# Performance work log

Hardware: AMD Instinct MI355X
Metric: run time of the kernel (lower is better)

## Reference

```python
import jax, jax.numpy as jnp
import numpy as np

N = 100_000   # nodes
E = 1_600_000 # edges
F_IN = 256    # num_features
HID = 128     # hidden_channels * heads
G = 128       # graphs in batch
C = 2         # num_classes
BN_EPS = 1e-5


def setup_inputs() -> dict:
    key = jax.random.key(0)
    ks = jax.random.split(key, 12)
    x = jax.random.normal(ks[0], (N, F_IN), dtype=jnp.float32)
    edge_index = jax.random.randint(ks[1], (2, E), 0, N, dtype=jnp.int64)
    batch = jnp.sort(jax.random.randint(ks[2], (N,), 0, G, dtype=jnp.int64))
    s1 = 1.0 / np.sqrt(F_IN)
    s2 = 1.0 / np.sqrt(HID)
    W1 = jax.random.uniform(ks[3], (F_IN, HID), jnp.float32, -s1, s1)
    b1 = jnp.zeros((HID,), jnp.float32)
    W2 = jax.random.uniform(ks[4], (HID, HID), jnp.float32, -s2, s2)
    b2 = jnp.zeros((HID,), jnp.float32)
    W3 = jax.random.uniform(ks[5], (HID, HID), jnp.float32, -s2, s2)
    b3 = jnp.zeros((HID,), jnp.float32)
    bn_gamma = jnp.ones((HID,), jnp.float32)
    bn_beta = jnp.zeros((HID,), jnp.float32)
    bn_mean = jnp.zeros((HID,), jnp.float32)
    bn_var = jnp.ones((HID,), jnp.float32)
    lin_w = jax.random.uniform(ks[6], (HID, C), jnp.float32, -s2, s2)
    lin_b = jax.random.uniform(ks[7], (C,), jnp.float32, -s2, s2)
    return {
        "x": x, "edge_index": edge_index, "_": 0, "batch": batch,
        "W1": W1, "b1": b1, "W2": W2, "b2": b2, "W3": W3, "b3": b3,
        "bn_gamma": bn_gamma, "bn_beta": bn_beta,
        "bn_mean": bn_mean, "bn_var": bn_var,
        "lin_w": lin_w, "lin_b": lin_b,
    }


def reference(x, edge_index, _, batch, W1, b1, W2, b2, W3, b3,
              bn_gamma, bn_beta, bn_mean, bn_var, lin_w, lin_b):
    src, dst = edge_index[0], edge_index[1]
    # GCN symmetric normalization with self-loops (gcn_norm):
    # deg[i] = 1 + in_degree(i); norm_e = deg[src]^-1/2 * deg[dst]^-1/2
    deg = 1.0 + jax.ops.segment_sum(jnp.ones((E,), x.dtype), dst, num_segments=N)
    dis = jax.lax.rsqrt(deg)
    norm_e = (dis[src] * dis[dst])[:, None]        # [E,1]
    self_norm = (1.0 / deg)[:, None]               # [N,1] self-loop weight

    def gcn_conv(h, W, b):
        hw = h @ W                                  # transform first (PyG order)
        agg = jax.ops.segment_sum(hw[src] * norm_e, dst, num_segments=N)
        return agg + hw * self_norm + b

    h = jax.nn.relu(gcn_conv(x, W1, b1))
    h = jax.nn.relu(gcn_conv(h, W2, b2))
    h = jax.nn.relu(gcn_conv(h, W3, b3))

    # global_mean_pool over graph ids
    counts = jax.ops.segment_sum(jnp.ones((N,), h.dtype), batch, num_segments=G)
    pooled = jax.ops.segment_sum(h, batch, num_segments=G) / jnp.maximum(counts, 1.0)[:, None]

    # dropout p=0.5 is identity in eval mode; BatchNorm1d with running stats
    xb = (pooled - bn_mean) * jax.lax.rsqrt(bn_var + BN_EPS) * bn_gamma + bn_beta
    out = jax.nn.relu(xb @ lin_w + lin_b)
    return (xb, out)
```

## Files before the change

### kernel.cpp

```cpp
#include <hip/hip_runtime.h>

#define NNODES 100000
#define NEDGES 1600000
#define FIN 256
#define HID 128
#define NG 128
#define NB 391
#define NW 256
#define EPW 6250
#define GEMM_BLKS 1563

static constexpr float BN_EPS_C = 1e-5f;

typedef __attribute__((ext_vector_type(8))) short bf16x8;
typedef __attribute__((ext_vector_type(4))) float f32x4;
typedef __attribute__((ext_vector_type(2))) float f32x2;

#if defined(__has_builtin)
#if __has_builtin(__builtin_amdgcn_cvt_pk_f32_fp8)
#define HAS_HWFP8 1
#endif
#endif

__device__ __forceinline__ float b2f(unsigned short u) {
    union { unsigned int i; float f; } c; c.i = ((unsigned int)u) << 16; return c.f;
}
__device__ __forceinline__ unsigned short f2b(float f) {
    union { float f; unsigned int i; } c; c.f = f;
    unsigned int u = c.i;
    u += 0x7fffu + ((u >> 16) & 1u);
    return (unsigned short)(u >> 16);
}

__device__ __forceinline__ unsigned char f2e8(float f) {
    union { float f; unsigned int u; } c; c.f = f;
    unsigned int s = (c.u >> 24) & 0x80u;
    c.u &= 0x7fffffffu;
    c.f = fminf(fmaxf(c.f, 0.015625f), 448.f);
    unsigned int u = c.u + 0x7ffffu + ((c.u >> 20) & 1u);
    int e = (int)(u >> 23) - 127;
    unsigned int m = (u >> 20) & 7u;
    return (unsigned char)(s | ((unsigned int)(e + 7) << 3) | m);
}

__device__ __forceinline__ float e8byte(unsigned int b) {
    union { unsigned int u; float f; } c;
    c.u = ((b & 0x80u) << 24) | (0x3C000000u + ((b & 0x7fu) << 20));
    return c.f;
}
__device__ __forceinline__ f32x2 e8plo(unsigned int w) {
#ifdef HAS_HWFP8
    return __builtin_amdgcn_cvt_pk_f32_fp8(w, false);
#else
    f32x2 r; r[0] = e8byte(w & 0xffu); r[1] = e8byte((w >> 8) & 0xffu); return r;
#endif
}
__device__ __forceinline__ f32x2 e8phi(unsigned int w) {
#ifdef HAS_HWFP8
    return __builtin_amdgcn_cvt_pk_f32_fp8(w, true);
#else
    f32x2 r; r[0] = e8byte((w >> 16) & 0xffu); r[1] = e8byte(w >> 24); return r;
#endif
}
__device__ __forceinline__ f32x2 bdec(unsigned int u) {
    union { unsigned int i[2]; f32x2 f; } c;
    c.i[0] = u << 16;
    c.i[1] = u & 0xffff0000u;
    return c.f;
}

__device__ __forceinline__ int aswz(int g) { return g ^ ((g >> 4) & 3); }

template<int K, int MODE, int OUT8>
__device__ __forceinline__ void gemm_body(int blk,
                                          const void* __restrict__ Araw,
                                          const unsigned short* __restrict__ whl,
                                          void* __restrict__ hwbv) {
    __shared__ __align__(16) unsigned short Ah0[2048];
    __shared__ __align__(16) unsigned short Ah1[2048];
    __shared__ __align__(16) unsigned short Bs[8192];

    const int tid = threadIdx.x;
    const int w = tid >> 6;
    const int lane = tid & 63;
    const int m0 = blk * 64;
    const int ar = tid >> 2;
    const int ak = (tid & 3) * 8;
    const int adst = aswz(((ar >> 4) * 64) + (ar & 15) + 16 * (ak >> 3)) * 8;
    const int ards = aswz(w * 64 + lane) * 8;

    f32x4 acc[8] = {};

    for (int kt = 0; kt < K; kt += 32) {
        if (MODE == 0) {
            const float* A = (const float*)Araw;
            float4 v0 = {0.f,0.f,0.f,0.f}, v1 = {0.f,0.f,0.f,0.f};
            int grow = m0 + ar;
            if (grow < NNODES) {
                const float* s = A + (size_t)grow * K + kt + ak;
                v0 = *(const float4*)(s);
                v1 = *(const float4*)(s + 4);
            }
            float av[8];
            *(float4*)(av) = v0; *(float4*)(av + 4) = v1;
            bf16x8 hv, lv;
            #pragma unroll
            for (int j = 0; j < 8; ++j) {
                unsigned short h = f2b(av[j]);
                hv[j] = (short)h;
                lv[j] = (short)f2b(av[j] - b2f(h));
            }
            *(bf16x8*)&Ah0[adst] = hv;
            *(bf16x8*)&Ah1[adst] = lv;
        } else {
            const unsigned short* A = (const unsigned short*)Araw;
            bf16x8 hv = {};
            int grow = m0 + ar;
            if (grow < NNODES)
                hv = *(const bf16x8*)(A + (size_t)grow * K + kt + ak);
            *(bf16x8*)&Ah0[adst] = hv;
        }
        {
            const float4* bsrc = (const float4*)(whl + (size_t)(kt >> 5) * 8192);
            float4* bdst = (float4*)Bs;
            #pragma unroll
            for (int i = 0; i < 4; ++i) bdst[tid * 4 + i] = bsrc[tid * 4 + i];
        }
        __syncthreads();
        bf16x8 a0 = *(const bf16x8*)&Ah0[ards];
        bf16x8 a1;
        if (MODE == 0) a1 = *(const bf16x8*)&Ah1[ards];
        #pragma unroll
        for (int t = 0; t < 8; ++t) {
            bf16x8 b0 = *(const bf16x8*)&Bs[(t * 64 + lane) * 8];
            bf16x8 b1 = *(const bf16x8*)&Bs[4096 + (t * 64 + lane) * 8];
            acc[t] = __builtin_amdgcn_mfma_f32_16x16x32_bf16(a0, b0, acc[t], 0, 0, 0);
            acc[t] = __builtin_amdgcn_mfma_f32_16x16x32_bf16(a0, b1, acc[t], 0, 0, 0);
            if (MODE == 0)
                acc[t] = __builtin_amdgcn_mfma_f32_16x16x32_bf16(a1, b0, acc[t], 0, 0, 0);
        }
        __syncthreads();
    }

    const int colLo = lane & 15;
    const int gq = lane >> 4;
    #pragma unroll
    for (int i = 0; i < 4; ++i) {
        int row = m0 + w * 16 + gq * 4 + i;
        if (row < NNODES) {
            #pragma unroll
            for (int t = 0; t < 8; ++t) {
                int col = t * 16 + colLo;
                float v = acc[t][i];
                if (OUT8) {
                    ((unsigned char*)hwbv)[(size_t)row * HID + col] = f2e8(v * 64.f);
                } else {
                    ((unsigned short*)hwbv)[(size_t)row * HID + col] = f2b(v);
                }
            }
        }
    }
}

__global__ __launch_bounds__(256) void k_prep(const float* __restrict__ W1,
                                              const float* __restrict__ W2,
                                              const float* __restrict__ W3,
                                              unsigned short* __restrict__ whl1,
                                              unsigned short* __restrict__ whl2,
                                              unsigned short* __restrict__ whl3,
                                              const int* __restrict__ dst,
                                              int* __restrict__ hist) {
    if (blockIdx.x < 256) {
        int idx = blockIdx.x * 256 + threadIdx.x;
        const float* W; unsigned short* whl;
        if (idx < FIN * 128) { W = W1; whl = whl1; }
        else if (idx < (FIN + HID) * 128) { W = W2; whl = whl2; idx -= FIN * 128; }
        else { W = W3; whl = whl3; idx -= (FIN + HID) * 128; }
        int k = idx >> 7, c = idx & 127;
        float v = W[k * 128 + c];
        unsigned short hi = f2b(v);
        unsigned short lo = f2b(v - b2f(hi));
        int kstep = k >> 5, kk = k & 31, g = kk >> 3, j = kk & 7;
        int tile = c >> 4, lane = (c & 15) + 16 * g;
        size_t b0 = ((((size_t)kstep * 2 + 0) * 8 + tile) * 64 + lane) * 8 + j;
        size_t b1 = ((((size_t)kstep * 2 + 1) * 8 + tile) * 64 + lane) * 8 + j;
        whl[b0] = hi;
        whl[b1] = lo;
    } else {
        __shared__ int h[NB];
        int w = blockIdx.x - 256, t = threadIdx.x;
        for (int i = t; i < NB; i += 256) h[i] = 0;
        __syncthreads();
        int base = w * EPW;
        for (int i = t; i < EPW; i += 256) atomicAdd(&h[dst[base + i] >> 8], 1);
        __syncthreads();
        for (int i = t; i < NB; i += 256) hist[i * NW + w] = h[i];
    }
}

__global__ __launch_bounds__(256) void kbB2(const int* __restrict__ hist,
                                            int* __restrict__ off,
                                            int* __restrict__ btot) {
    __shared__ int s[NW];
    int b = blockIdx.x, t = threadIdx.x;
    int v = hist[b * NW + t];
    s[t] = v;
    __syncthreads();
    for (int o = 1; o < NW; o <<= 1) {
        int a = (t >= o) ? s[t - o] : 0;
        __syncthreads();
        s[t] += a;
        __syncthreads();
    }
    off[b * NW + t] = s[t] - v;
    if (t == NW - 1) btot[b] = s[t];
}

__global__ __launch_bounds__(512) void kbT(const int* __restrict__ btot,
                                           int* __restrict__ bbase,
                                           int* __restrict__ rowptr) {
    __shared__ int s[512];
    int t = threadIdx.x;
    int v = (t < NB) ? btot[t] : 0;
    s[t] = v;
    __syncthreads();
    for (int o = 1; o < 512; o <<= 1) {
        int a = (t >= o) ? s[t - o] : 0;
        __syncthreads();
        s[t] += a;
        __syncthreads();
    }
    if (t < NB) bbase[t] = s[t] - v;
    if (t == NB - 1) { bbase[NB] = s[t]; rowptr[NNODES] = NEDGES; }
}

__global__ __launch_bounds__(256) void k_c2g1(const int* __restrict__ src,
                                              const int* __restrict__ dst,
                                              const int* __restrict__ off,
                                              const int* __restrict__ bbase,
                                              int* __restrict__ pairs,
                                              const float* __restrict__ x,
                                              const unsigned short* __restrict__ whl1,
                                              void* __restrict__ hwbv) {
    if (blockIdx.x < 256) {
        __shared__ int cur[NB];
        int w = blockIdx.x, t = threadIdx.x;
        for (int i = t; i < NB; i += 256) cur[i] = off[i * NW + w] + bbase[i];
        __syncthreads();
        int base = w * EPW;
        for (int i = t; i < EPW; i += 256) {
            int d = dst[base + i];
            int pos = atomicAdd(&cur[d >> 8], 1);
            pairs[pos] = (src[base + i] << 8) | (d & 255);
        }
    } else {
        gemm_body<FIN, 0, 1>(blockIdx.x - 256, x, whl1, hwbv);
    }
}

__global__ __launch_bounds__(256) void kb2y(const int* __restrict__ bbase,
                                            const int* __restrict__ pairs,
                                            int* __restrict__ rowptr,
                                            float* __restrict__ dis,
                                            float* __restrict__ selfn) {
    int b = blockIdx.x;
    int nbase = b * 256;
    int nmax = NNODES - nbase; if (nmax > 256) nmax = 256;
    __shared__ int cnt[256];
    __shared__ int cur[256];
    int t = threadIdx.x;
    cnt[t] = 0;
    __syncthreads();
    int beg = bbase[b], end = bbase[b + 1];
    for (int i = beg + t; i < end; i += 256) atomicAdd(&cnt[pairs[i] & 255], 1);
    __syncthreads();
    int v = cnt[t];
    cur[t] = v;
    __syncthreads();
    for (int o = 1; o < 256; o <<= 1) {
        int a = (t >= o) ? cur[t - o] : 0;
        __syncthreads();
        cur[t] += a;
        __syncthreads();
    }
    if (t < nmax) {
        rowptr[nbase + t] = cur[t] - v + beg;
        float d = 1.0f + (float)v;
        dis[nbase + t] = rsqrtf(d);
        selfn[nbase + t] = 1.0f / d;
    }
}

__global__ __launch_bounds__(256) void kb2z(const int* __restrict__ bbase,
                                            const int* __restrict__ pairs,
                                            const int* __restrict__ rowptr,
                                            const float* __restrict__ dis,
                                            unsigned int* __restrict__ edgp) {
    int b = blockIdx.x;
    int nbase = b * 256;
    int nmax = NNODES - nbase; if (nmax > 256) nmax = 256;
    __shared__ int cur[256];
    __shared__ float disl[256];
    int t = threadIdx.x;
    if (t < nmax) {
        cur[t] = rowptr[nbase + t];
        disl[t] = dis[nbase + t];
    }
    __syncthreads();
    int beg = bbase[b], end = bbase[b + 1];
    for (int i = beg + t; i < end; i += 256) {
        int p = pairs[i];
        int s = p >> 8;
        float w = dis[s] * disl[p & 255];
        unsigned int u = (unsigned int)(w * 32767.f + 0.5f);
        int pos = atomicAdd(&cur[p & 255], 1);
        edgp[pos] = ((unsigned int)s << 15) | u;
    }
}

template<int K, int MODE, int OUT8>
__global__ __launch_bounds__(256) void k_gemm_mfma(const void* __restrict__ Araw,
                                                   const unsigned short* __restrict__ whl,
                                                   void* __restrict__ hwbv) {
    gemm_body<K, MODE, OUT8>(blockIdx.x, Araw, whl, hwbv);
}

template<int IN8>
__global__ __launch_bounds__(256) void k_gather(const int* __restrict__ rowptr,
                                                const unsigned int* __restrict__ edgp,
                                                const void* __restrict__ hwbv,
                                                const float* __restrict__ selfn,
                                                const float* __restrict__ bias,
                                                unsigned short* __restrict__ agb) {
    const int lane = threadIdx.x & 63;
    const int sub = lane >> 4;
    const int l4 = lane & 15;
    const int node = blockIdx.x * 16 + ((threadIdx.x >> 6) << 2) + sub;
    int beg = rowptr[node], end = rowptr[node + 1];
    const float q = IN8 ? (1.0f / (32767.0f * 64.0f)) : (1.0f / 32767.0f);
    const unsigned char* hb = (const unsigned char*)hwbv;
    f32x2 a0 = {0.f,0.f}, a1 = {0.f,0.f}, a2 = {0.f,0.f}, a3 = {0.f,0.f};
    int e = beg;
    if (IN8) {
        for (; e + 7 < end; e += 8) {
            unsigned int p0 = edgp[e], p1 = edgp[e + 1];
            unsigned int p2 = edgp[e + 2], p3 = edgp[e + 3];
            unsigned int p4 = edgp[e + 4], p5 = edgp[e + 5];
            unsigned int p6 = edgp[e + 6], p7 = edgp[e + 7];
            uint2 v0 = *(const uint2*)(hb + (size_t)(p0 >> 15) * HID + l4 * 8);
            uint2 v1 = *(const uint2*)(hb + (size_t)(p1 >> 15) * HID + l4 * 8);
            uint2 v2 = *(const uint2*)(hb + (size_t)(p2 >> 15) * HID + l4 * 8);
            uint2 v3 = *(const uint2*)(hb + (size_t)(p3 >> 15) * HID + l4 * 8);
            uint2 v4 = *(const uint2*)(hb + (size_t)(p4 >> 15) * HID + l4 * 8);
            uint2 v5 = *(const uint2*)(hb + (size_t)(p5 >> 15) * HID + l4 * 8);
            uint2 v6 = *(const uint2*)(hb + (size_t)(p6 >> 15) * HID + l4 * 8);
            uint2 v7 = *(const uint2*)(hb + (size_t)(p7 >> 15) * HID + l4 * 8);
            float w0 = (float)(p0 & 0x7fffu) * q, w1 = (float)(p1 & 0x7fffu) * q;
            float w2 = (float)(p2 & 0x7fffu) * q, w3 = (float)(p3 & 0x7fffu) * q;
            float w4 = (float)(p4 & 0x7fffu) * q, w5 = (float)(p5 & 0x7fffu) * q;
            float w6 = (float)(p6 & 0x7fffu) * q, w7 = (float)(p7 & 0x7fffu) * q;
            f32x2 wa = {w0, w0}, wb = {w1, w1}, wc = {w2, w2}, wd = {w3, w3};
            f32x2 we = {w4, w4}, wf = {w5, w5}, wg = {w6, w6}, wh = {w7, w7};
            a0 += e8plo(v0.x) * wa; a1 += e8phi(v0.x) * wa;
            a2 += e8plo(v0.y) * wa; a3 += e8phi(v0.y) * wa;
            a0 += e8plo(v1.x) * wb; a1 += e8phi(v1.x) * wb;
            a2 += e8plo(v1.y) * wb; a3 += e8phi(v1.y) * wb;
            a0 += e8plo(v2.x) * wc; a1 += e8phi(v2.x) * wc;
            a2 += e8plo(v2.y) * wc; a3 += e8phi(v2.y) * wc;
            a0 += e8plo(v3.x) * wd; a1 += e8phi(v3.x) * wd;
            a2 += e8plo(v3.y) * wd; a3 += e8phi(v3.y) * wd;
            a0 += e8plo(v4.x) * we; a1 += e8phi(v4.x) * we;
            a2 += e8plo(v4.y) * we; a3 += e8phi(v4.y) * we;
            a0 += e8plo(v5.x) * wf; a1 += e8phi(v5.x) * wf;
            a2 += e8plo(v5.y) * wf; a3 += e8phi(v5.y) * wf;
            a0 += e8plo(v6.x) * wg; a1 += e8phi(v6.x) * wg;
            a2 += e8plo(v6.y) * wg; a3 += e8phi(v6.y) * wg;
            a0 += e8plo(v7.x) * wh; a1 += e8phi(v7.x) * wh;
            a2 += e8plo(v7.y) * wh; a3 += e8phi(v7.y) * wh;
        }
    } else {
        for (; e + 3 < end; e += 4) {
            unsigned int p0 = edgp[e], p1 = edgp[e + 1];
            unsigned int p2 = edgp[e + 2], p3 = edgp[e + 3];
            float w0 = (float)(p0 & 0x7fffu) * q;
            float w1 = (float)(p1 & 0x7fffu) * q;
            float w2 = (float)(p2 & 0x7fffu) * q;
            float w3 = (float)(p3 & 0x7fffu) * q;
            f32x2 wa = {w0, w0}, wb = {w1, w1}, wc = {w2, w2}, wd = {w3, w3};
            size_t r0 = (size_t)(p0 >> 15), r1 = (size_t)(p1 >> 15);
            size_t r2 = (size_t)(p2 >> 15), r3 = (size_t)(p3 >> 15);
            uint4 v0 = *(const uint4*)(hb + r0 * (HID * 2) + l4 * 16);
            uint4 v1 = *(const uint4*)(hb + r1 * (HID * 2) + l4 * 16);
            uint4 v2 = *(const uint4*)(hb + r2 * (HID * 2) + l4 * 16);
            uint4 v3 = *(const uint4*)(hb + r3 * (HID * 2) + l4 * 16);
            a0 += bdec(v0.x) * wa; a1 += bdec(v0.y) * wa;
            a2 += bdec(v0.z) * wa; a3 += bdec(v0.w) * wa;
            a0 += bdec(v1.x) * wb; a1 += bdec(v1.y) * wb;
            a2 += bdec(v1.z) * wb; a3 += bdec(v1.w) * wb;
            a0 += bdec(v2.x) * wc; a1 += bdec(v2.y) * wc;
            a2 += bdec(v2.z) * wc; a3 += bdec(v2.w) * wc;
            a0 += bdec(v3.x) * wd; a1 += bdec(v3.y) * wd;
            a2 += bdec(v3.z) * wd; a3 += bdec(v3.w) * wd;
        }
    }
    for (; e < end; ++e) {
        unsigned int p = edgp[e];
        float w = (float)(p & 0x7fffu) * q;
        f32x2 wa = {w, w};
        size_t r = (size_t)(p >> 15);
        if (IN8) {
            uint2 v = *(const uint2*)(hb + r * HID + l4 * 8);
            a0 += e8plo(v.x) * wa; a1 += e8phi(v.x) * wa;
            a2 += e8plo(v.y) * wa; a3 += e8phi(v.y) * wa;
        } else {
            uint4 v = *(const uint4*)(hb + r * (HID * 2) + l4 * 16);
            a0 += bdec(v.x) * wa; a1 += bdec(v.y) * wa;
            a2 += bdec(v.z) * wa; a3 += bdec(v.w) * wa;
        }
    }
    float sn = selfn[node] * (IN8 ? (1.0f / 64.0f) : 1.0f);
    f32x2 sn2 = {sn, sn};
    f32x2 h0, h1, h2, h3;
    if (IN8) {
        uint2 v = *(const uint2*)(hb + (size_t)node * HID + l4 * 8);
        h0 = e8plo(v.x); h1 = e8phi(v.x); h2 = e8plo(v.y); h3 = e8phi(v.y);
    } else {
        uint4 v = *(const uint4*)(hb + (size_t)node * (HID * 2) + l4 * 16);
        h0 = bdec(v.x); h1 = bdec(v.y); h2 = bdec(v.z); h3 = bdec(v.w);
    }
    float4 bA = *(const float4*)&bias[l4 * 8];
    float4 bB = *(const float4*)&bias[l4 * 8 + 4];
    a0 += h0 * sn2; a1 += h1 * sn2; a2 += h2 * sn2; a3 += h3 * sn2;
    float r0 = fmaxf(a0[0] + bA.x, 0.f), r1 = fmaxf(a0[1] + bA.y, 0.f);
    float r2 = fmaxf(a1[0] + bA.z, 0.f), r3 = fmaxf(a1[1] + bA.w, 0.f);
    float r4 = fmaxf(a2[0] + bB.x, 0.f), r5 = fmaxf(a2[1] + bB.y, 0.f);
    float r6 = fmaxf(a3[0] + bB.z, 0.f), r7 = fmaxf(a3[1] + bB.w, 0.f);
    uint4 o;
    o.x = (unsigned int)f2b(r0) | ((unsigned int)f2b(r1) << 16);
    o.y = (unsigned int)f2b(r2) | ((unsigned int)f2b(r3) << 16);
    o.z = (unsigned int)f2b(r4) | ((unsigned int)f2b(r5) << 16);
    o.w = (unsigned int)f2b(r6) | ((unsigned int)f2b(r7) << 16);
    *(uint4*)(agb + (size_t)node * HID + l4 * 8) = o;
}

__global__ __launch_bounds__(1024) void k_pool_bn_head(const unsigned short* __restrict__ h,
                                                       const int* __restrict__ batch,
                                                       const float* __restrict__ gamma,
                                                       const float* __restrict__ beta,
                                                       const float* __restrict__ mean,
                                                       const float* __restrict__ var,
                                                       const float* __restrict__ lw,
                                                       const float* __restrict__ lb,
                                                       float* __restrict__ xb,
                                                       float* __restrict__ out2) {
    int g = blockIdx.x;
    int tid = threadIdx.x;
    int fg = tid & 15;
    int r = tid >> 4;
    __shared__ int bounds[2];
    if (tid < 2) {
        int target = g + tid;
        int a = 0, b = NNODES;
        while (a < b) { int m = (a + b) >> 1; if (batch[m] < target) a = m + 1; else b = m; }
        bounds[tid] = a;
    }
    __syncthreads();
    int s1 = bounds[0], e1 = bounds[1];
    f32x2 acc[4] = {};
    for (int i = s1 + r; i < e1; i += 64) {
        uint4 v = *(const uint4*)(h + (size_t)i * HID + fg * 8);
        acc[0] += bdec(v.x); acc[1] += bdec(v.y); acc[2] += bdec(v.z); acc[3] += bdec(v.w);
    }
    __shared__ f32x2 red[64][16][4];
    #pragma unroll
    for (int j = 0; j < 4; ++j) red[r][fg][j] = acc[j];
    __syncthreads();
    for (int off = 32; off >= 1; off >>= 1) {
        if (r < off) {
            #pragma unroll
            for (int j = 0; j < 4; ++j) red[r][fg][j] += red[r + off][fg][j];
        }
        __syncthreads();
    }
    __shared__ float xbl[128];
    if (r == 0) {
        float cnt = (float)((e1 - s1) > 0 ? (e1 - s1) : 1);
        float inv = 1.0f / cnt;
        #pragma unroll
        for (int j = 0; j < 4; ++j) {
            #pragma unroll
            for (int k2 = 0; k2 < 2; ++k2) {
                int f = fg * 8 + j * 2 + k2;
                float pooled = red[0][fg][j][k2] * inv;
                float xbv = (pooled - mean[f]) * rsqrtf(var[f] + BN_EPS_C) * gamma[f] + beta[f];
                xb[g * HID + f] = xbv;
                xbl[f] = xbv;
            }
        }
    }
    __syncthreads();
    if (tid < 64) {
        float x0 = xbl[tid], x1 = xbl[tid + 64];
        float s0 = x0 * lw[tid * 2 + 0] + x1 * lw[(tid + 64) * 2 + 0];
        float s1h = x0 * lw[tid * 2 + 1] + x1 * lw[(tid + 64) * 2 + 1];
        #pragma unroll
        for (int o = 1; o < 64; o <<= 1) {
            s0 += __shfl_xor(s0, o);
            s1h += __shfl_xor(s1h, o);
        }
        if (tid == 0) {
            out2[g * 2 + 0] = fmaxf(s0 + lb[0], 0.f);
            out2[g * 2 + 1] = fmaxf(s1h + lb[1], 0.f);
        }
    }
}

extern "C" void kernel_launch(void* const* d_in, const int* in_sizes, int n_in,
                              void* d_out, int out_size, void* d_ws, size_t ws_size,
                              hipStream_t stream) {
    const float* x     = (const float*)d_in[0];
    const int*   ei    = (const int*)d_in[1];
    const int*   batch = (const int*)d_in[3];
    const float* W1 = (const float*)d_in[4];
    const float* b1 = (const float*)d_in[5];
    const float* W2 = (const float*)d_in[6];
    const float* b2 = (const float*)d_in[7];
    const float* W3 = (const float*)d_in[8];
    const float* b3 = (const float*)d_in[9];
    const float* gamma = (const float*)d_in[10];
    const float* beta  = (const float*)d_in[11];
    const float* mean  = (const float*)d_in[12];
    const float* var   = (const float*)d_in[13];
    const float* lw = (const float*)d_in[14];
    const float* lb = (const float*)d_in[15];
    float* out = (float*)d_out;

    char* p = (char*)d_ws;
    unsigned short* HWB = (unsigned short*)p;          p += (size_t)NNODES * HID * 2;
    unsigned short* AGB = (unsigned short*)p;          p += (size_t)NNODES * HID * 2;
    float* DIS    = (float*)p;                         p += (size_t)NNODES * 4;
    float* SELFN  = (float*)p;                         p += (size_t)NNODES * 4;
    int*   ROWPTR = (int*)p;                           p += (size_t)(NNODES + 64) * 4;
    unsigned int* EDGP = (unsigned int*)p;             p += (size_t)NEDGES * 4;
    int*   PAIRS  = (int*)p;                           p += (size_t)NEDGES * 4;
    int*   BTOT   = (int*)p;                           p += 512 * 4;
    int*   BBASE  = (int*)p;                           p += 512 * 4;
    unsigned short* WHL1 = (unsigned short*)p;         p += (size_t)FIN * 128 * 2 * 2;
    unsigned short* WHL2 = (unsigned short*)p;         p += (size_t)HID * 128 * 2 * 2;
    unsigned short* WHL3 = (unsigned short*)p;
    int*   HIST   = (int*)AGB;
    int*   OFF    = HIST + NB * NW;

    const int* srcv = ei;
    const int* dstv = ei + NEDGES;

    k_prep<<<512, 256, 0, stream>>>(W1, W2, W3, WHL1, WHL2, WHL3, dstv, HIST);
    kbB2<<<NB, 256, 0, stream>>>(HIST, OFF, BTOT);
    kbT<<<1, 512, 0, stream>>>(BTOT, BBASE, ROWPTR);
    k_c2g1<<<256 + GEMM_BLKS, 256, 0, stream>>>(srcv, dstv, OFF, BBASE, PAIRS, x, WHL1, HWB);
    kb2y<<<NB, 256, 0, stream>>>(BBASE, PAIRS, ROWPTR, DIS, SELFN);
    kb2z<<<NB, 256, 0, stream>>>(BBASE, PAIRS, ROWPTR, DIS, EDGP);

    const int ggat = NNODES / 16;
    dim3 gg(GEMM_BLKS);

    k_gather<1><<<ggat, 256, 0, stream>>>(ROWPTR, EDGP, HWB, SELFN, b1, AGB);
    k_gemm_mfma<HID, 1, 1><<<gg, 256, 0, stream>>>(AGB, WHL2, HWB);
    k_gather<1><<<ggat, 256, 0, stream>>>(ROWPTR, EDGP, HWB, SELFN, b2, AGB);
    k_gemm_mfma<HID, 1, 0><<<gg, 256, 0, stream>>>(AGB, WHL3, HWB);
    k_gather<0><<<ggat, 256, 0, stream>>>(ROWPTR, EDGP, HWB, SELFN, b3, AGB);

    k_pool_bn_head<<<NG, 1024, 0, stream>>>(AGB, batch, gamma, beta, mean, var,
                                            lw, lb, out, out + (size_t)NG * HID);
}
```

Baseline: 260.4 us.

## Use single-pass bf16 GEMM for layer 1 and interleave scatter blocks with GEMM blocks

Adds a MODE 2 GEMM path for the first layer that converts x to bf16 once and issues one MFMA per tile. It drops the hi/lo split of A and the second weight half, cutting MFMA count and LDS traffic by about two thirds. It also spreads the 256 edge-scatter blocks evenly among the GEMM blocks (every 7th block) rather than placing them first, so the two workloads share the CUs more evenly. Dropping the compensation terms lowers layer-1 precision, which risks accuracy against the fp32 reference.

```diff
diff --git a/kernel.cpp b/kernel.cpp
--- a/kernel.cpp
+++ b/kernel.cpp
@@ -77,8 +77,8 @@
                                           const unsigned short* __restrict__ whl,
                                           void* __restrict__ hwbv) {
     __shared__ __align__(16) unsigned short Ah0[2048];
-    __shared__ __align__(16) unsigned short Ah1[2048];
-    __shared__ __align__(16) unsigned short Bs[8192];
+    __shared__ __align__(16) unsigned short Ah1[(MODE == 0) ? 2048 : 16];
+    __shared__ __align__(16) unsigned short Bs[(MODE == 2) ? 4096 : 8192];
 
     const int tid = threadIdx.x;
     const int w = tid >> 6;
@@ -92,7 +92,7 @@
     f32x4 acc[8] = {};
 
     for (int kt = 0; kt < K; kt += 32) {
-        if (MODE == 0) {
+        if (MODE == 0 || MODE == 2) {
             const float* A = (const float*)Araw;
             float4 v0 = {0.f,0.f,0.f,0.f}, v1 = {0.f,0.f,0.f,0.f};
             int grow = m0 + ar;
@@ -103,15 +103,17 @@
             }
             float av[8];
             *(float4*)(av) = v0; *(float4*)(av + 4) = v1;
-            bf16x8 hv, lv;
+            bf16x8 hv;
             #pragma unroll
-            for (int j = 0; j < 8; ++j) {
-                unsigned short h = f2b(av[j]);
-                hv[j] = (short)h;
-                lv[j] = (short)f2b(av[j] - b2f(h));
+            for (int j = 0; j < 8; ++j) hv[j] = (short)f2b(av[j]);
+            *(bf16x8*)&Ah0[adst] = hv;
+            if (MODE == 0) {
+                bf16x8 lv;
+                #pragma unroll
+                for (int j = 0; j < 8; ++j)
+                    lv[j] = (short)f2b(av[j] - b2f((unsigned short)hv[j]));
+                *(bf16x8*)&Ah1[adst] = lv;
             }
-            *(bf16x8*)&Ah0[adst] = hv;
-            *(bf16x8*)&Ah1[adst] = lv;
         } else {
             const unsigned short* A = (const unsigned short*)Araw;
             bf16x8 hv = {};
@@ -123,8 +125,13 @@
         {
             const float4* bsrc = (const float4*)(whl + (size_t)(kt >> 5) * 8192);
             float4* bdst = (float4*)Bs;
-            #pragma unroll
-            for (int i = 0; i < 4; ++i) bdst[tid * 4 + i] = bsrc[tid * 4 + i];
+            if (MODE == 2) {
+                #pragma unroll
+                for (int i = 0; i < 2; ++i) bdst[tid * 2 + i] = bsrc[tid * 2 + i];
+            } else {
+                #pragma unroll
+                for (int i = 0; i < 4; ++i) bdst[tid * 4 + i] = bsrc[tid * 4 + i];
+            }
         }
         __syncthreads();
         bf16x8 a0 = *(const bf16x8*)&Ah0[ards];
@@ -133,11 +140,13 @@
         #pragma unroll
         for (int t = 0; t < 8; ++t) {
             bf16x8 b0 = *(const bf16x8*)&Bs[(t * 64 + lane) * 8];
-            bf16x8 b1 = *(const bf16x8*)&Bs[4096 + (t * 64 + lane) * 8];
             acc[t] = __builtin_amdgcn_mfma_f32_16x16x32_bf16(a0, b0, acc[t], 0, 0, 0);
-            acc[t] = __builtin_amdgcn_mfma_f32_16x16x32_bf16(a0, b1, acc[t], 0, 0, 0);
-            if (MODE == 0)
-                acc[t] = __builtin_amdgcn_mfma_f32_16x16x32_bf16(a1, b0, acc[t], 0, 0, 0);
+            if (MODE != 2) {
+                bf16x8 b1 = *(const bf16x8*)&Bs[4096 + (t * 64 + lane) * 8];
+                acc[t] = __builtin_amdgcn_mfma_f32_16x16x32_bf16(a0, b1, acc[t], 0, 0, 0);
+                if (MODE == 0)
+                    acc[t] = __builtin_amdgcn_mfma_f32_16x16x32_bf16(a1, b0, acc[t], 0, 0, 0);
+            }
         }
         __syncthreads();
     }
@@ -242,9 +251,10 @@
                                               const float* __restrict__ x,
                                               const unsigned short* __restrict__ whl1,
                                               void* __restrict__ hwbv) {
-    if (blockIdx.x < 256) {
+    int b = blockIdx.x;
+    if ((b % 7 == 0) && (b / 7 < 256)) {
         __shared__ int cur[NB];
-        int w = blockIdx.x, t = threadIdx.x;
+        int w = b / 7, t = threadIdx.x;
         for (int i = t; i < NB; i += 256) cur[i] = off[i * NW + w] + bbase[i];
         __syncthreads();
         int base = w * EPW;
@@ -254,7 +264,8 @@
             pairs[pos] = (src[base + i] << 8) | (d & 255);
         }
     } else {
-        gemm_body<FIN, 0, 1>(blockIdx.x - 256, x, whl1, hwbv);
+        int sbefore = (b + 6) / 7; if (sbefore > 256) sbefore = 256;
+        gemm_body<FIN, 2, 1>(b - sbefore, x, whl1, hwbv);
     }
 }
 
```

Result: faster. 255.3 us (median of 2 runs) (-2.0%).
